# Kernel optimization log

Measured on AMD Instinct MI355X. Metric: run time of the kernel, lower is better.

## Reference

```python
import jax, jax.numpy as jnp
import numpy as np

B, S, DM = 2, 2048, 1024  # batch, seq_len, model_dim
H, HD = 16, 64            # num_heads, head_dim (H*HD == DM)


def setup_inputs() -> dict:
    key = jax.random.key(0)
    ks = jax.random.split(key, 8)
    scale = 0.02
    return {
        "k": jax.random.normal(ks[0], (B, S, DM), jnp.float32),
        "q": jax.random.normal(ks[1], (B, S, DM), jnp.float32),
        "v": jax.random.normal(ks[2], (B, S, DM), jnp.float32),
        "Wk": jax.random.normal(ks[3], (DM, H * HD), jnp.float32) * scale,
        "bk": jnp.zeros((H * HD,), jnp.float32),
        "Wq": jax.random.normal(ks[4], (DM, H * HD), jnp.float32) * scale,
        "bq": jnp.zeros((H * HD,), jnp.float32),
        "Wv": jax.random.normal(ks[5], (DM, H * HD), jnp.float32) * scale,
        "bv": jnp.zeros((H * HD,), jnp.float32),
        "Wo": jax.random.normal(ks[6], (H * HD, DM), jnp.float32) * scale,
        "bo": jnp.zeros((DM,), jnp.float32),
    }


def reference(k, q, v, Wk, bk, Wq, bq, Wv, bv, Wo, bo):
    # QKV projections (Dense with bias)
    kp = (k @ Wk + bk).reshape(B, S, H, HD)
    qp = (q @ Wq + bq).reshape(B, S, H, HD)
    vp = (v @ Wv + bv).reshape(B, S, H, HD)
    # Faithful to original: scores indexed [b, key_c, h, query_q],
    # softmax over the QUERY axis, NO 1/sqrt(head_dim) scaling.
    scores = jnp.einsum('bchd,bqhd->bchq', kp, qp)
    attn = jax.nn.softmax(scores, axis=-1)
    out = jnp.einsum('bchq,bqhd->bchd', attn, vp)  # [B, S(keys), H, HD]
    out = out.reshape(B, S, H * HD)
    return out @ Wo + bo
```

## Files before the change

kernel.cpp:

```cpp
#include <hip/hip_runtime.h>
#include <hip/hip_bf16.h>
#include <stdint.h>
#include <stddef.h>


typedef __attribute__((ext_vector_type(4))) float f32x4;
typedef __attribute__((ext_vector_type(16))) float f32x16;
typedef __attribute__((ext_vector_type(8))) short s16x8;
typedef __attribute__((ext_vector_type(4))) unsigned int u32x4;
typedef __attribute__((ext_vector_type(4))) unsigned short u16x4;

#define DEV static __device__ __forceinline__

DEV unsigned short f2bf(float x) {
  unsigned int u = __float_as_uint(x);
  u += 0x7FFF + ((u >> 16) & 1);
  return (unsigned short)(u >> 16);
}
DEV f32x4 mfma16(s16x8 a, s16x8 b, f32x4 c) {
  return __builtin_amdgcn_mfma_f32_16x16x32_bf16(a, b, c, 0, 0, 0);
}
DEV f32x16 mfma32(s16x8 a, s16x8 b, f32x16 c) {
  return __builtin_amdgcn_mfma_f32_32x32x16_bf16(a, b, c, 0, 0, 0);
}
DEV f32x4 fzero() { f32x4 z; z[0]=0.f; z[1]=0.f; z[2]=0.f; z[3]=0.f; return z; }
DEV f32x16 fzero16() {
  f32x16 z;
#pragma unroll
  for (int i = 0; i < 16; ++i) z[i] = 0.f;
  return z;
}
DEV float fexp2(float x) { return __builtin_amdgcn_exp2f(x); }

DEV void gload_lds16(const unsigned short* g, unsigned short* l) {
  __builtin_amdgcn_global_load_lds(
      (const __attribute__((address_space(1))) unsigned int*)g,
      (__attribute__((address_space(3))) unsigned int*)l, 16, 0, 0);
}

#define CVTPK(dst, a, b) \
  asm("v_cvt_pk_bf16_f32 %0, %1, %2" : "=v"(dst) : "v"(a), "v"(b))
#define PSWAP(x, y) \
  asm("v_permlane32_swap_b32 %0, %1" : "+v"(x), "+v"(y))

struct CvtArgs { const float* x[3]; unsigned short* y[3]; };

__global__ __launch_bounds__(256) void cvt_kernel(CvtArgs a) {
  const float* x = a.x[blockIdx.y];
  unsigned short* y = a.y[blockIdx.y];
  const int i = blockIdx.x * 256 + threadIdx.x;
  f32x4 v = ((const f32x4*)x)[i];
  u16x4 o;
#pragma unroll
  for (int j = 0; j < 4; ++j) o[j] = f2bf(v[j]);
  ((u16x4*)y)[i] = o;
}

struct WArgs { const float* W[4]; unsigned short* Wt[4]; };

__global__ __launch_bounds__(256) void wtrans_kernel(WArgs a) {
  const float* W = a.W[blockIdx.z];
  unsigned short* Wt = a.Wt[blockIdx.z];
  const int n0 = blockIdx.x * 32, k0 = blockIdx.y * 32;
  __shared__ float t[32][33];
  const int tx = threadIdx.x & 31, ty = threadIdx.x >> 5;
#pragma unroll
  for (int i = 0; i < 4; ++i)
    t[ty + i*8][tx] = W[(size_t)(k0 + ty + i*8) * 1024 + n0 + tx];
  __syncthreads();
#pragma unroll
  for (int i = 0; i < 4; ++i)
    Wt[(size_t)(n0 + ty + i*8) * 1024 + k0 + tx] = f2bf(t[tx][ty + i*8]);
}

struct GemArgs {
  const unsigned short* A[3];
  const unsigned short* Wt[3];
  const float* bias[3];
  void* C[3];
  int mode[3];
  float scale[3];
};

template<int BM>
__global__ __launch_bounds__(256) void gemm_kernel(GemArgs g) {
  constexpr int MF = BM / 32;
  const int z = blockIdx.z;
  const unsigned short* A  = g.A[z];
  const unsigned short* Wt = g.Wt[z];
  const float* bias = g.bias[z];
  const int mode = g.mode[z];
  const float scale = g.scale[z];
  const int m0 = blockIdx.y * BM, n0 = blockIdx.x * 128;
  const int tid = threadIdx.x;
  const int lane = tid & 63, w = tid >> 6;
  const int wm = w >> 1, wn = w & 1;
  const int lg = lane >> 4, lr = lane & 15, lx = lr & 7;

  __shared__ __align__(16) unsigned short As[BM * 64];
  __shared__ __align__(16) unsigned short Bs[128 * 64];

  f32x4 acc[MF][4];
#pragma unroll
  for (int i = 0; i < MF; ++i)
#pragma unroll
    for (int j = 0; j < 4; ++j) acc[i][j] = fzero();

  const int aStep = (mode == 2) ? 2048 * 64 : 64;
  const unsigned short* srcA[MF]; unsigned short* dstA[MF];
#pragma unroll
  for (int c = 0; c < MF; ++c) {
    int n = c*256 + tid, row = n >> 3, cg = (n & 7) ^ (row & 7);
    int s = m0 + row;
    size_t abase = (mode == 2)
        ? ((size_t)((s >> 11) * 16) * 2048 + (s & 2047)) * 64 + cg * 8
        : (size_t)s * 1024 + cg * 8;
    srcA[c] = A + abase;
    dstA[c] = &As[n * 8];
  }
  const unsigned short* srcB[4]; unsigned short* dstB[4];
#pragma unroll
  for (int c = 0; c < 4; ++c) {
    int n = c*256 + tid, row = n >> 3, cg = (n & 7) ^ (row & 7);
    srcB[c] = Wt + (size_t)(n0 + row) * 1024 + cg * 8;
    dstB[c] = &Bs[n * 8];
  }

  for (int it = 0; it < 16; ++it) {
    __syncthreads();
#pragma unroll
    for (int c = 0; c < MF; ++c) { gload_lds16(srcA[c], dstA[c]); srcA[c] += aStep; }
#pragma unroll
    for (int c = 0; c < 4; ++c)  { gload_lds16(srcB[c], dstB[c]); srcB[c] += 64; }
    __syncthreads();

    s16x8 af[2][MF], bf[2][4];
#pragma unroll
    for (int ks = 0; ks < 2; ++ks) {
#pragma unroll
      for (int mf = 0; mf < MF; ++mf) {
        int row = wm*(BM/2) + mf*16 + lr;
        af[ks][mf] = *(const s16x8*)&As[row*64 + ((ks*4 + lg) ^ lx) * 8];
      }
#pragma unroll
      for (int nf = 0; nf < 4; ++nf) {
        int row = wn*64 + nf*16 + lr;
        bf[ks][nf] = *(const s16x8*)&Bs[row*64 + ((ks*4 + lg) ^ lx) * 8];
      }
    }
#pragma unroll
    for (int mf = 0; mf < MF; ++mf)
#pragma unroll
      for (int nf = 0; nf < 4; ++nf) {
        acc[mf][nf] = mfma16(af[0][mf], bf[0][nf], acc[mf][nf]);
        acc[mf][nf] = mfma16(af[1][mf], bf[1][nf], acc[mf][nf]);
      }
  }

#pragma unroll
  for (int nf = 0; nf < 4; ++nf) {
    const int colg = n0 + wn*64 + nf*16 + lr;
    const float bi = bias[colg];
#pragma unroll
    for (int mf = 0; mf < MF; ++mf) {
      const int rowg0 = m0 + wm*(BM/2) + mf*16 + lg*4;
      if (mode == 0) {
        unsigned short* o = (unsigned short*)g.C[z];
#pragma unroll
        for (int r = 0; r < 4; ++r)
          o[(size_t)(rowg0 + r) * 1024 + colg] = f2bf((acc[mf][nf][r] + bi) * scale);
      } else if (mode == 1) {
        const int hh = colg >> 6, d = colg & 63;
        const int bb2 = rowg0 >> 11, s = rowg0 & 2047;
        u16x4 pk;
#pragma unroll
        for (int r = 0; r < 4; ++r) pk[r] = f2bf(acc[mf][nf][r] + bi);
        *(u16x4*)((unsigned short*)g.C[z] + ((size_t)((bb2*16 + hh)*64 + d)) * 2048 + s) = pk;
      } else {
        float* o = (float*)g.C[z];
#pragma unroll
        for (int r = 0; r < 4; ++r)
          o[(size_t)(rowg0 + r) * 1024 + colg] = acc[mf][nf][r] + bi;
      }
    }
  }
}

__global__ __launch_bounds__(256) void attn_kernel(
    const unsigned short* __restrict__ kp, const unsigned short* __restrict__ qp,
    const unsigned short* __restrict__ vpt, unsigned short* __restrict__ aout) {
  const int F = blockIdx.x;
  const int swz = (F & 7) * 64 + (F >> 3);
  const int bh = swz >> 4, cblk = swz & 15;
  const int b = bh >> 4, h = bh & 15;
  const int c0 = cblk * 128;
  const int tid = threadIdx.x, lane = tid & 63, w = tid >> 6;
  const int cg = w & 1, jg = w >> 1;
  const int ln = lane & 31, hh = lane >> 5;

  __shared__ __align__(16) unsigned short qa_lds[2][2][2048];
  __shared__ __align__(16) unsigned short vb_lds[2][2][2048];
  __shared__ float lbuf[2][2][64];

  const int srow = tid >> 3, sp = tid & 7, sl = sp ^ (srow & 7);
  const unsigned short* qsrc0 =
      qp + (size_t)(b*2048 + srow) * 1024 + h*64 + sl*8;
  const unsigned short* qsrc1 = qsrc0 + (size_t)1024 * 1024;
  const int sd = srow + 32*(sl >> 2), sjc = sl & 3;
  const unsigned short* vsrc0 =
      vpt + ((size_t)((b*16 + h)*64) + sd) * 2048 + sjc*8;
  const unsigned short* vsrc1 = vsrc0 + 1024;

  s16x8 kbA[4], kbB[4];
  {
    const unsigned short* krowA =
        kp + (size_t)(b*2048 + c0 + cg*64 + ln) * 1024 + h*64 + hh*8;
    const unsigned short* krowB = krowA + 32 * 1024;
#pragma unroll
    for (int s = 0; s < 4; ++s) {
      kbA[s] = *(const s16x8*)(krowA + s*16);
      kbB[s] = *(const s16x8*)(krowB + s*16);
    }
  }

  f32x16 accA0 = fzero16(), accA1 = fzero16();
  f32x16 accB0 = fzero16(), accB1 = fzero16();
  float lA = 0.f, lB = 0.f;

  gload_lds16(qsrc0, &qa_lds[0][0][tid*8]);
  gload_lds16(qsrc1, &qa_lds[0][1][tid*8]);
  gload_lds16(vsrc0, &vb_lds[0][0][tid*8]);
  gload_lds16(vsrc1, &vb_lds[0][1][tid*8]);
  qsrc0 += 32*1024; qsrc1 += 32*1024; vsrc0 += 32; vsrc1 += 32;
  __syncthreads();

  for (int jt = 0; jt < 32; ++jt) {
    const int cur = jt & 1;
    if (jt + 1 < 32) {
      gload_lds16(qsrc0, &qa_lds[cur^1][0][tid*8]);
      gload_lds16(qsrc1, &qa_lds[cur^1][1][tid*8]);
      gload_lds16(vsrc0, &vb_lds[cur^1][0][tid*8]);
      gload_lds16(vsrc1, &vb_lds[cur^1][1][tid*8]);
      qsrc0 += 32*1024; qsrc1 += 32*1024; vsrc0 += 32; vsrc1 += 32;
    }

    s16x8 qa0, qa1, qa2, qa3;
    {
      const unsigned short* base = &qa_lds[cur][jg][0];
      qa0 = *(const s16x8*)&base[(ln*8 + ((0 + hh) ^ (ln & 7)))*8];
      qa1 = *(const s16x8*)&base[(ln*8 + ((2 + hh) ^ (ln & 7)))*8];
      qa2 = *(const s16x8*)&base[(ln*8 + ((4 + hh) ^ (ln & 7)))*8];
      qa3 = *(const s16x8*)&base[(ln*8 + ((6 + hh) ^ (ln & 7)))*8];
    }
    s16x8 vb0, vb1, vb2, vb3;
    {
      const unsigned short* base = &vb_lds[cur][jg][0];
      vb0 = *(const s16x8*)&base[(ln*8 + ((0 + hh) ^ (ln & 7)))*8];
      vb1 = *(const s16x8*)&base[(ln*8 + ((2 + hh) ^ (ln & 7)))*8];
      vb2 = *(const s16x8*)&base[(ln*8 + ((4 + hh) ^ (ln & 7)))*8];
      vb3 = *(const s16x8*)&base[(ln*8 + ((6 + hh) ^ (ln & 7)))*8];
    }

    f32x16 scA = fzero16(), scB = fzero16();
    __builtin_amdgcn_s_setprio(1);
    scA = mfma32(qa0, kbA[0], scA); scA = mfma32(qa1, kbA[1], scA);
    scA = mfma32(qa2, kbA[2], scA); scA = mfma32(qa3, kbA[3], scA);
    scB = mfma32(qa0, kbB[0], scB); scB = mfma32(qa1, kbB[1], scB);
    scB = mfma32(qa2, kbB[2], scB); scB = mfma32(qa3, kbB[3], scB);
    __builtin_amdgcn_s_setprio(0);

#define SOFTMAX_PV(SC, LRUN, ACC0, ACC1)                                      \
  {                                                                           \
    _Pragma("unroll")                                                         \
    for (int r = 0; r < 16; ++r) SC[r] = fexp2(SC[r]);                        \
    {                                                                         \
      float t0 = (SC[0] + SC[1]) + (SC[2] + SC[3]);                           \
      float t1 = (SC[4] + SC[5]) + (SC[6] + SC[7]);                           \
      float t2 = (SC[8] + SC[9]) + (SC[10] + SC[11]);                         \
      float t3 = (SC[12] + SC[13]) + (SC[14] + SC[15]);                       \
      LRUN += (t0 + t1) + (t2 + t3);                                          \
    }                                                                         \
    unsigned int a0, a1, b0, b1;                                              \
    u32x4 wv; s16x8 pa0, pa1;                                                 \
    CVTPK(a0, SC[0], SC[1]);  CVTPK(b0, SC[4], SC[5]);  PSWAP(a0, b0);        \
    CVTPK(a1, SC[2], SC[3]);  CVTPK(b1, SC[6], SC[7]);  PSWAP(a1, b1);        \
    wv[0] = a0; wv[1] = a1; wv[2] = b0; wv[3] = b1;                           \
    pa0 = __builtin_bit_cast(s16x8, wv);                                      \
    CVTPK(a0, SC[8], SC[9]);  CVTPK(b0, SC[12], SC[13]); PSWAP(a0, b0);       \
    CVTPK(a1, SC[10], SC[11]); CVTPK(b1, SC[14], SC[15]); PSWAP(a1, b1);      \
    wv[0] = a0; wv[1] = a1; wv[2] = b0; wv[3] = b1;                           \
    pa1 = __builtin_bit_cast(s16x8, wv);                                      \
    __builtin_amdgcn_s_setprio(1);                                            \
    ACC0 = mfma32(vb0, pa0, ACC0);                                            \
    ACC0 = mfma32(vb1, pa1, ACC0);                                            \
    ACC1 = mfma32(vb2, pa0, ACC1);                                            \
    ACC1 = mfma32(vb3, pa1, ACC1);                                            \
    __builtin_amdgcn_s_setprio(0);                                            \
  }

    SOFTMAX_PV(scA, lA, accA0, accA1);
    SOFTMAX_PV(scB, lB, accB0, accB1);
#undef SOFTMAX_PV

    __syncthreads();
  }

  float* mrg = cg ? (float*)&vb_lds[0][0][0] : (float*)&qa_lds[0][0][0];
  if (jg == 1) {
    lbuf[cg][0][lane] = lA; lbuf[cg][1][lane] = lB;
#pragma unroll
    for (int r = 0; r < 16; ++r) {
      mrg[(r)*64 + lane]      = accA0[r];
      mrg[(16 + r)*64 + lane] = accA1[r];
      mrg[(32 + r)*64 + lane] = accB0[r];
      mrg[(48 + r)*64 + lane] = accB1[r];
    }
  }
  __syncthreads();
  if (jg == 0) {
    lA += lbuf[cg][0][lane]; lB += lbuf[cg][1][lane];
#pragma unroll
    for (int r = 0; r < 16; ++r) {
      accA0[r] += mrg[(r)*64 + lane];
      accA1[r] += mrg[(16 + r)*64 + lane];
      accB0[r] += mrg[(32 + r)*64 + lane];
      accB1[r] += mrg[(48 + r)*64 + lane];
    }
    lA += __shfl_xor(lA, 32);
    lB += __shfl_xor(lB, 32);
    const float invA = 1.0f / lA, invB = 1.0f / lB;
    unsigned short* obaseA =
        aout + ((size_t)bh * 2048 + c0 + cg*64 + ln) * 64 + hh * 4;
    unsigned short* obaseB = obaseA + 32 * 64;
#pragma unroll
    for (int dt = 0; dt < 2; ++dt)
#pragma unroll
      for (int rq = 0; rq < 4; ++rq) {
        u16x4 pkA, pkB;
#pragma unroll
        for (int i = 0; i < 4; ++i) {
          const int reg = rq*4 + i;
          pkA[i] = f2bf(((dt == 0) ? accA0[reg] : accA1[reg]) * invA);
          pkB[i] = f2bf(((dt == 0) ? accB0[reg] : accB1[reg]) * invB);
        }
        *(u16x4*)(obaseA + dt*32 + rq*8) = pkA;
        *(u16x4*)(obaseB + dt*32 + rq*8) = pkB;
      }
  }
}

extern "C" void kernel_launch(void* const* d_in, const int* in_sizes, int n_in,
                              void* d_out, int out_size, void* d_ws, size_t ws_size,
                              hipStream_t stream) {
  (void)in_sizes; (void)n_in; (void)out_size; (void)ws_size;
  const float* k  = (const float*)d_in[0];
  const float* q  = (const float*)d_in[1];
  const float* v  = (const float*)d_in[2];
  const float* Wk = (const float*)d_in[3];
  const float* bk = (const float*)d_in[4];
  const float* Wq = (const float*)d_in[5];
  const float* bq = (const float*)d_in[6];
  const float* Wv = (const float*)d_in[7];
  const float* bv = (const float*)d_in[8];
  const float* Wo = (const float*)d_in[9];
  const float* bo = (const float*)d_in[10];

  char* ws = (char*)d_ws;
  const size_t MB = 1024 * 1024;
  unsigned short* Wkt = (unsigned short*)(ws + 0*MB);
  unsigned short* Wqt = (unsigned short*)(ws + 2*MB);
  unsigned short* Wvt = (unsigned short*)(ws + 4*MB);
  unsigned short* Wot = (unsigned short*)(ws + 6*MB);
  unsigned short* kp  = (unsigned short*)(ws + 8*MB);
  unsigned short* qp  = (unsigned short*)(ws + 16*MB);
  unsigned short* vpt = (unsigned short*)(ws + 24*MB);
  unsigned short* vc  = (unsigned short*)(ws + 32*MB);
  unsigned short* aoutb = (unsigned short*)(ws + 40*MB);
  unsigned short* kc = (unsigned short*)d_out;
  unsigned short* qc = (unsigned short*)((char*)d_out + 8*MB);

  CvtArgs ca;
  ca.x[0] = k; ca.x[1] = q; ca.x[2] = v;
  ca.y[0] = kc; ca.y[1] = qc; ca.y[2] = vc;
  cvt_kernel<<<dim3(4096, 3), 256, 0, stream>>>(ca);

  WArgs wa;
  wa.W[0] = Wk; wa.W[1] = Wq; wa.W[2] = Wv; wa.W[3] = Wo;
  wa.Wt[0] = Wkt; wa.Wt[1] = Wqt; wa.Wt[2] = Wvt; wa.Wt[3] = Wot;
  wtrans_kernel<<<dim3(32, 32, 4), 256, 0, stream>>>(wa);

  GemArgs gp;
  gp.A[0] = kc; gp.A[1] = qc; gp.A[2] = vc;
  gp.Wt[0] = Wkt; gp.Wt[1] = Wqt; gp.Wt[2] = Wvt;
  gp.bias[0] = bk; gp.bias[1] = bq; gp.bias[2] = bv;
  gp.C[0] = kp; gp.C[1] = qp; gp.C[2] = vpt;
  gp.mode[0] = 0; gp.mode[1] = 0; gp.mode[2] = 1;
  gp.scale[0] = 1.4426950408889634f;
  gp.scale[1] = 1.0f; gp.scale[2] = 1.0f;
  gemm_kernel<128><<<dim3(8, 32, 3), 256, 0, stream>>>(gp);

  attn_kernel<<<dim3(512), 256, 0, stream>>>(kp, qp, vpt, aoutb);

  GemArgs gf;
  gf.A[0] = aoutb; gf.A[1] = aoutb; gf.A[2] = aoutb;
  gf.Wt[0] = Wot; gf.Wt[1] = Wot; gf.Wt[2] = Wot;
  gf.bias[0] = bo; gf.bias[1] = bo; gf.bias[2] = bo;
  gf.C[0] = d_out; gf.C[1] = d_out; gf.C[2] = d_out;
  gf.mode[0] = 2; gf.mode[1] = 2; gf.mode[2] = 2;
  gf.scale[0] = 1.0f; gf.scale[1] = 1.0f; gf.scale[2] = 1.0f;
  gemm_kernel<64><<<dim3(8, 64, 1), 256, 0, stream>>>(gf);
}
```

Measured before the change: 135.0 us.

## Give each wave private LDS staging buffers and drop per-iteration block barriers

Replaces the block-shared double-buffered Q/V staging with per-wave buffers that each wave fills with its own global-to-LDS loads. Each wave now walks its own half of the query range directly, so the per-iteration __syncthreads is replaced by wave-local waitcnt plus sched_barrier. V is single-buffered and reloaded right after it is read into registers. This removes block-wide synchronisation stalls, but duplicates Q/V loads across the two cg waves that share a jg, doubling global/L2 traffic and LDS footprint. It also drains vmcnt at the end of each iteration, which limits how far loads can overlap compute.

```diff
diff --git a/kernel.cpp b/kernel.cpp
--- a/kernel.cpp
+++ b/kernel.cpp
@@ -198,18 +198,24 @@
   const int cg = w & 1, jg = w >> 1;
   const int ln = lane & 31, hh = lane >> 5;
 
-  __shared__ __align__(16) unsigned short qa_lds[2][2][2048];
-  __shared__ __align__(16) unsigned short vb_lds[2][2][2048];
+  __shared__ __align__(16) unsigned short qa_lds[4][2][2048];
+  __shared__ __align__(16) unsigned short vb_lds[4][2048];
   __shared__ float lbuf[2][2][64];
 
-  const int srow = tid >> 3, sp = tid & 7, sl = sp ^ (srow & 7);
-  const unsigned short* qsrc0 =
-      qp + (size_t)(b*2048 + srow) * 1024 + h*64 + sl*8;
-  const unsigned short* qsrc1 = qsrc0 + (size_t)1024 * 1024;
-  const int sd = srow + 32*(sl >> 2), sjc = sl & 3;
-  const unsigned short* vsrc0 =
-      vpt + ((size_t)((b*16 + h)*64) + sd) * 2048 + sjc*8;
-  const unsigned short* vsrc1 = vsrc0 + 1024;
+  const unsigned short* qsrc[4];
+  const unsigned short* vsrc[4];
+  unsigned short* qdst[2][4];
+  unsigned short* vdst[4];
+#pragma unroll
+  for (int c = 0; c < 4; ++c) {
+    const int n = c*64 + lane, row = n >> 3, sp = n & 7, sl = sp ^ (row & 7);
+    qsrc[c] = qp + (size_t)(b*2048 + jg*1024 + row) * 1024 + h*64 + sl*8;
+    const int sd = row + 32*(sl >> 2), sjc = sl & 3;
+    vsrc[c] = vpt + ((size_t)((b*16 + h)*64) + sd) * 2048 + jg*1024 + sjc*8;
+    qdst[0][c] = &qa_lds[w][0][n * 8];
+    qdst[1][c] = &qa_lds[w][1][n * 8];
+    vdst[c] = &vb_lds[w][n * 8];
+  }
 
   s16x8 kbA[4], kbB[4];
   {
@@ -227,26 +233,20 @@
   f32x16 accB0 = fzero16(), accB1 = fzero16();
   float lA = 0.f, lB = 0.f;
 
-  gload_lds16(qsrc0, &qa_lds[0][0][tid*8]);
-  gload_lds16(qsrc1, &qa_lds[0][1][tid*8]);
-  gload_lds16(vsrc0, &vb_lds[0][0][tid*8]);
-  gload_lds16(vsrc1, &vb_lds[0][1][tid*8]);
-  qsrc0 += 32*1024; qsrc1 += 32*1024; vsrc0 += 32; vsrc1 += 32;
-  __syncthreads();
+#pragma unroll
+  for (int c = 0; c < 4; ++c) {
+    gload_lds16(qsrc[c], qdst[0][c]); qsrc[c] += 32*1024;
+    gload_lds16(vsrc[c], vdst[c]);    vsrc[c] += 32;
+  }
+  asm volatile("s_waitcnt vmcnt(0)" ::: "memory");
+  __builtin_amdgcn_sched_barrier(0);
 
   for (int jt = 0; jt < 32; ++jt) {
     const int cur = jt & 1;
-    if (jt + 1 < 32) {
-      gload_lds16(qsrc0, &qa_lds[cur^1][0][tid*8]);
-      gload_lds16(qsrc1, &qa_lds[cur^1][1][tid*8]);
-      gload_lds16(vsrc0, &vb_lds[cur^1][0][tid*8]);
-      gload_lds16(vsrc1, &vb_lds[cur^1][1][tid*8]);
-      qsrc0 += 32*1024; qsrc1 += 32*1024; vsrc0 += 32; vsrc1 += 32;
-    }
 
     s16x8 qa0, qa1, qa2, qa3;
     {
-      const unsigned short* base = &qa_lds[cur][jg][0];
+      const unsigned short* base = &qa_lds[w][cur][0];
       qa0 = *(const s16x8*)&base[(ln*8 + ((0 + hh) ^ (ln & 7)))*8];
       qa1 = *(const s16x8*)&base[(ln*8 + ((2 + hh) ^ (ln & 7)))*8];
       qa2 = *(const s16x8*)&base[(ln*8 + ((4 + hh) ^ (ln & 7)))*8];
@@ -254,11 +254,21 @@
     }
     s16x8 vb0, vb1, vb2, vb3;
     {
-      const unsigned short* base = &vb_lds[cur][jg][0];
+      const unsigned short* base = &vb_lds[w][0];
       vb0 = *(const s16x8*)&base[(ln*8 + ((0 + hh) ^ (ln & 7)))*8];
       vb1 = *(const s16x8*)&base[(ln*8 + ((2 + hh) ^ (ln & 7)))*8];
       vb2 = *(const s16x8*)&base[(ln*8 + ((4 + hh) ^ (ln & 7)))*8];
       vb3 = *(const s16x8*)&base[(ln*8 + ((6 + hh) ^ (ln & 7)))*8];
+    }
+    asm volatile("s_waitcnt lgkmcnt(0)" ::: "memory");
+    __builtin_amdgcn_sched_barrier(0);
+
+    if (jt + 1 < 32) {
+#pragma unroll
+      for (int c = 0; c < 4; ++c) {
+        gload_lds16(qsrc[c], qdst[cur^1][c]); qsrc[c] += 32*1024;
+        gload_lds16(vsrc[c], vdst[c]);        vsrc[c] += 32;
+      }
     }
 
     f32x16 scA = fzero16(), scB = fzero16();
@@ -302,10 +312,12 @@
     SOFTMAX_PV(scB, lB, accB0, accB1);
 #undef SOFTMAX_PV
 
-    __syncthreads();
-  }
-
-  float* mrg = cg ? (float*)&vb_lds[0][0][0] : (float*)&qa_lds[0][0][0];
+    asm volatile("s_waitcnt vmcnt(0)" ::: "memory");
+    __builtin_amdgcn_sched_barrier(0);
+  }
+
+  __syncthreads();
+  float* mrg = cg ? (float*)&vb_lds[0][0] : (float*)&qa_lds[0][0][0];
   if (jg == 1) {
     lbuf[cg][0][lane] = lA; lbuf[cg][1][lane] = lB;
 #pragma unroll
```

New measurement: 147.8 us. 1.09x slower.

## Split attention query loop across four wave groups with 512-thread blocks

Applied to the files above, without the earlier changes.

The attention kernel now runs 512 threads per block, splitting the query sweep into four interleaved quarter-ranges per key tile instead of two, so each wave group iterates 16 times instead of 32. Shared Q/V staging doubles, and partial accumulators and row sums are combined through a multi-step LDS reduction with several extra barriers. This aims to raise waves per CU and shorten the serial loop, at the cost of more LDS per block, a longer merge phase, and possibly lower block occupancy.

```diff
diff --git a/kernel.cpp b/kernel.cpp
--- a/kernel.cpp
+++ b/kernel.cpp
@@ -186,7 +186,7 @@
   }
 }
 
-__global__ __launch_bounds__(256) void attn_kernel(
+__global__ __launch_bounds__(512) void attn_kernel(
     const unsigned short* __restrict__ kp, const unsigned short* __restrict__ qp,
     const unsigned short* __restrict__ vpt, unsigned short* __restrict__ aout) {
   const int F = blockIdx.x;
@@ -195,21 +195,24 @@
   const int b = bh >> 4, h = bh & 15;
   const int c0 = cblk * 128;
   const int tid = threadIdx.x, lane = tid & 63, w = tid >> 6;
-  const int cg = w & 1, jg = w >> 1;
+  const int cg = w & 1, jq = w >> 1;
   const int ln = lane & 31, hh = lane >> 5;
 
-  __shared__ __align__(16) unsigned short qa_lds[2][2][2048];
-  __shared__ __align__(16) unsigned short vb_lds[2][2][2048];
-  __shared__ float lbuf[2][2][64];
-
-  const int srow = tid >> 3, sp = tid & 7, sl = sp ^ (srow & 7);
-  const unsigned short* qsrc0 =
-      qp + (size_t)(b*2048 + srow) * 1024 + h*64 + sl*8;
-  const unsigned short* qsrc1 = qsrc0 + (size_t)1024 * 1024;
-  const int sd = srow + 32*(sl >> 2), sjc = sl & 3;
-  const unsigned short* vsrc0 =
-      vpt + ((size_t)((b*16 + h)*64) + sd) * 2048 + sjc*8;
-  const unsigned short* vsrc1 = vsrc0 + 1024;
+  __shared__ __align__(16) unsigned short qa_lds[2][4][2048];
+  __shared__ __align__(16) unsigned short vb_lds[2][4][2048];
+
+  const unsigned short* qsrc[2];
+  const unsigned short* vsrc[2];
+  int qoff[2];
+#pragma unroll
+  for (int c2 = 0; c2 < 2; ++c2) {
+    const int n = c2*512 + tid, jqs = n >> 8, m = n & 255;
+    const int row = m >> 3, sp = m & 7, sl = sp ^ (row & 7);
+    qsrc[c2] = qp + (size_t)(b*2048 + jqs*512 + row) * 1024 + h*64 + sl*8;
+    const int sd = row + 32*(sl >> 2), sjc = sl & 3;
+    vsrc[c2] = vpt + ((size_t)((b*16 + h)*64) + sd) * 2048 + jqs*512 + sjc*8;
+    qoff[c2] = jqs*2048 + m*8;
+  }
 
   s16x8 kbA[4], kbB[4];
   {
@@ -227,26 +230,26 @@
   f32x16 accB0 = fzero16(), accB1 = fzero16();
   float lA = 0.f, lB = 0.f;
 
-  gload_lds16(qsrc0, &qa_lds[0][0][tid*8]);
-  gload_lds16(qsrc1, &qa_lds[0][1][tid*8]);
-  gload_lds16(vsrc0, &vb_lds[0][0][tid*8]);
-  gload_lds16(vsrc1, &vb_lds[0][1][tid*8]);
-  qsrc0 += 32*1024; qsrc1 += 32*1024; vsrc0 += 32; vsrc1 += 32;
-  __syncthreads();
-
-  for (int jt = 0; jt < 32; ++jt) {
+#pragma unroll
+  for (int c2 = 0; c2 < 2; ++c2) {
+    gload_lds16(qsrc[c2], &qa_lds[0][0][0] + qoff[c2]); qsrc[c2] += 32*1024;
+    gload_lds16(vsrc[c2], &vb_lds[0][0][0] + qoff[c2]); vsrc[c2] += 32;
+  }
+  __syncthreads();
+
+  for (int jt = 0; jt < 16; ++jt) {
     const int cur = jt & 1;
-    if (jt + 1 < 32) {
-      gload_lds16(qsrc0, &qa_lds[cur^1][0][tid*8]);
-      gload_lds16(qsrc1, &qa_lds[cur^1][1][tid*8]);
-      gload_lds16(vsrc0, &vb_lds[cur^1][0][tid*8]);
-      gload_lds16(vsrc1, &vb_lds[cur^1][1][tid*8]);
-      qsrc0 += 32*1024; qsrc1 += 32*1024; vsrc0 += 32; vsrc1 += 32;
+    if (jt + 1 < 16) {
+#pragma unroll
+      for (int c2 = 0; c2 < 2; ++c2) {
+        gload_lds16(qsrc[c2], &qa_lds[cur^1][0][0] + qoff[c2]); qsrc[c2] += 32*1024;
+        gload_lds16(vsrc[c2], &vb_lds[cur^1][0][0] + qoff[c2]); vsrc[c2] += 32;
+      }
     }
 
     s16x8 qa0, qa1, qa2, qa3;
     {
-      const unsigned short* base = &qa_lds[cur][jg][0];
+      const unsigned short* base = &qa_lds[cur][jq][0];
       qa0 = *(const s16x8*)&base[(ln*8 + ((0 + hh) ^ (ln & 7)))*8];
       qa1 = *(const s16x8*)&base[(ln*8 + ((2 + hh) ^ (ln & 7)))*8];
       qa2 = *(const s16x8*)&base[(ln*8 + ((4 + hh) ^ (ln & 7)))*8];
@@ -254,7 +257,7 @@
     }
     s16x8 vb0, vb1, vb2, vb3;
     {
-      const unsigned short* base = &vb_lds[cur][jg][0];
+      const unsigned short* base = &vb_lds[cur][jq][0];
       vb0 = *(const s16x8*)&base[(ln*8 + ((0 + hh) ^ (ln & 7)))*8];
       vb1 = *(const s16x8*)&base[(ln*8 + ((2 + hh) ^ (ln & 7)))*8];
       vb2 = *(const s16x8*)&base[(ln*8 + ((4 + hh) ^ (ln & 7)))*8];
@@ -305,27 +308,44 @@
     __syncthreads();
   }
 
-  float* mrg = cg ? (float*)&vb_lds[0][0][0] : (float*)&qa_lds[0][0][0];
-  if (jg == 1) {
-    lbuf[cg][0][lane] = lA; lbuf[cg][1][lane] = lB;
-#pragma unroll
-    for (int r = 0; r < 16; ++r) {
-      mrg[(r)*64 + lane]      = accA0[r];
-      mrg[(16 + r)*64 + lane] = accA1[r];
-      mrg[(32 + r)*64 + lane] = accB0[r];
-      mrg[(48 + r)*64 + lane] = accB1[r];
-    }
-  }
-  __syncthreads();
-  if (jg == 0) {
-    lA += lbuf[cg][0][lane]; lB += lbuf[cg][1][lane];
-#pragma unroll
-    for (int r = 0; r < 16; ++r) {
-      accA0[r] += mrg[(r)*64 + lane];
-      accA1[r] += mrg[(16 + r)*64 + lane];
-      accB0[r] += mrg[(32 + r)*64 + lane];
-      accB1[r] += mrg[(48 + r)*64 + lane];
-    }
+  float* S = (float*)&qa_lds[0][0][0];
+  const int base = cg * (66*64);
+
+#define PUBLISH()                                                             \
+  {                                                                           \
+    S[base + 64*64 + lane] = lA; S[base + 65*64 + lane] = lB;                 \
+    _Pragma("unroll")                                                         \
+    for (int r = 0; r < 16; ++r) {                                            \
+      S[base + (r)*64 + lane]      = accA0[r];                                \
+      S[base + (16 + r)*64 + lane] = accA1[r];                                \
+      S[base + (32 + r)*64 + lane] = accB0[r];                                \
+      S[base + (48 + r)*64 + lane] = accB1[r];                                \
+    }                                                                         \
+  }
+#define ABSORB()                                                              \
+  {                                                                           \
+    lA += S[base + 64*64 + lane]; lB += S[base + 65*64 + lane];               \
+    _Pragma("unroll")                                                         \
+    for (int r = 0; r < 16; ++r) {                                            \
+      accA0[r] += S[base + (r)*64 + lane];                                    \
+      accA1[r] += S[base + (16 + r)*64 + lane];                               \
+      accB0[r] += S[base + (32 + r)*64 + lane];                               \
+      accB1[r] += S[base + (48 + r)*64 + lane];                               \
+    }                                                                         \
+  }
+
+  if (jq == 1) PUBLISH();
+  __syncthreads();
+  if (jq == 0) ABSORB();
+  __syncthreads();
+  if (jq == 3) PUBLISH();
+  __syncthreads();
+  if (jq == 2) ABSORB();
+  __syncthreads();
+  if (jq == 2) PUBLISH();
+  __syncthreads();
+  if (jq == 0) {
+    ABSORB();
     lA += __shfl_xor(lA, 32);
     lB += __shfl_xor(lB, 32);
     const float invA = 1.0f / lA, invB = 1.0f / lB;
@@ -347,6 +367,8 @@
         *(u16x4*)(obaseB + dt*32 + rq*8) = pkB;
       }
   }
+#undef PUBLISH
+#undef ABSORB
 }
 
 extern "C" void kernel_launch(void* const* d_in, const int* in_sizes, int n_in,
@@ -399,7 +421,7 @@
   gp.scale[1] = 1.0f; gp.scale[2] = 1.0f;
   gemm_kernel<128><<<dim3(8, 32, 3), 256, 0, stream>>>(gp);
 
-  attn_kernel<<<dim3(512), 256, 0, stream>>>(kp, qp, vpt, aoutb);
+  attn_kernel<<<dim3(512), 512, 0, stream>>>(kp, qp, vpt, aoutb);
 
   GemArgs gf;
   gf.A[0] = aoutb; gf.A[1] = aoutb; gf.A[2] = aoutb;
```

Result: slower. 141.5 us (+4.8%).
